# Kernel tuning notes

Measured on AMD Instinct MI355X. Metric: run time of the kernel, lower is better.

Reference implementation:

```python
import jax, jax.numpy as jnp
import numpy as np

N = 100000      # nodes
E = 1600000     # edges
R = 8           # relation types
D = 128         # in_dim = h_dim = out_dim

def setup_inputs() -> dict:
    key = jax.random.key(0)
    ks = jax.random.split(key, 10)
    feats = jax.random.normal(ks[0], (N, D), dtype=jnp.float32)
    src = jax.random.randint(ks[1], (E,), 0, N, dtype=jnp.int32)
    dst = jax.random.randint(ks[2], (E,), 0, N, dtype=jnp.int32)
    etype = jax.random.randint(ks[3], (E,), 0, R, dtype=jnp.int32)
    s = 0.05  # keep activations well-scaled
    W1 = jax.random.normal(ks[4], (R, D, D), dtype=jnp.float32) * s
    loop_w1 = jax.random.normal(ks[5], (D, D), dtype=jnp.float32) * s
    b1 = jnp.zeros((D,), dtype=jnp.float32)
    W2 = jax.random.normal(ks[6], (R, D, D), dtype=jnp.float32) * s
    loop_w2 = jax.random.normal(ks[7], (D, D), dtype=jnp.float32) * s
    b2 = jnp.zeros((D,), dtype=jnp.float32)
    return {"feats": feats, "W1": W1, "loop_w1": loop_w1, "b1": b1,
            "W2": W2, "loop_w2": loop_w2, "b2": b2,
            "src": src, "dst": dst, "etype": etype}

def _rel_conv(h, W, loop_w, b, src, dst, etype, relu):
    # Per-relation transform of all node features: [R, N, out]
    # (cheaper than gathering a per-edge [E, in, out] weight tensor)
    h_rel = jnp.einsum('ni,rio->rno', h, W)
    # Per-edge message = W_{etype(e)} @ h[src(e)] : [E, out]
    msg = h_rel[etype, src]
    # Sum-aggregate messages at destination nodes
    agg = jax.ops.segment_sum(msg, dst, num_segments=h.shape[0])
    out = agg + h @ loop_w + b  # self-loop + bias
    return jax.nn.relu(out) if relu else out

def reference(feats, W1, loop_w1, b1, W2, loop_w2, b2, src, dst, etype):
    # eval-mode forward: dropout is identity
    h = _rel_conv(feats, W1, loop_w1, b1, src, dst, etype, relu=True)
    h = _rel_conv(h, W2, loop_w2, b2, src, dst, etype, relu=False)
    return h
```

## Files before the change

### kernel.cpp

```cpp
#include <hip/hip_runtime.h>
#include <hip/hip_bf16.h>


#define D 128
#define KTOT 1152
#define KACC 1024
#define BK 32
#define BSH 9
#define BSZ 512
#define TILE 4096

typedef __attribute__((ext_vector_type(8))) __bf16 bf16x8;
typedef __attribute__((ext_vector_type(8))) unsigned short us8;
typedef __attribute__((ext_vector_type(4))) unsigned short us4;
typedef __attribute__((ext_vector_type(4))) float f32x4;

__device__ __forceinline__ unsigned short f2bf(float f) {
    union { float f; unsigned u; } v; v.f = f;
    unsigned r = v.u + 0x7FFF + ((v.u >> 16) & 1);
    return (unsigned short)(r >> 16);
}
__device__ __forceinline__ float bf2f(unsigned short u) {
    return __uint_as_float((unsigned)u << 16);
}

__device__ __forceinline__ int lds_off(int row, int c) {
    return row * 32 + ((c ^ ((row >> 1) & 3)) << 3);
}


__global__ __launch_bounds__(256) void histA_kernel(const int* __restrict__ dst,
                                                    int* __restrict__ bcnt, int E, int nbuck) {
    __shared__ int c[1024];
    int t = threadIdx.x;
    for (int i = t; i < nbuck; i += 256) c[i] = 0;
    __syncthreads();
    int stride = gridDim.x * 256;
    for (int e = blockIdx.x * 256 + t; e < E; e += stride)
        atomicAdd(&c[dst[e] >> BSH], 1);
    __syncthreads();
    for (int i = t; i < nbuck; i += 256)
        if (c[i]) atomicAdd(&bcnt[i], c[i]);
}

__global__ __launch_bounds__(1024) void scanA_kernel(const int* __restrict__ bcnt,
                                                     int* __restrict__ boffs,
                                                     int* __restrict__ bhead, int nbuck) {
    int t = threadIdx.x;
    int v = (t < nbuck) ? bcnt[t] : 0;
    int lane = t & 63, w = t >> 6;
    int inc = v;
    #pragma unroll
    for (int off = 1; off < 64; off <<= 1) {
        int n = __shfl_up(inc, off, 64);
        if (lane >= off) inc += n;
    }
    __shared__ int ws[16];
    if (lane == 63) ws[w] = inc;
    __syncthreads();
    int wbase = 0;
    for (int i = 0; i < w; ++i) wbase += ws[i];
    int ex = wbase + inc - v;
    if (t < nbuck) { boffs[t] = ex; bhead[t] = ex; }
    if (t == nbuck - 1) boffs[nbuck] = ex + v;
}

__global__ __launch_bounds__(1024) void scatterA_kernel(const int* __restrict__ src,
                                                        const int* __restrict__ dst,
                                                        const int* __restrict__ et,
                                                        int* __restrict__ bhead,
                                                        int* __restrict__ sortedA, int E, int nbuck) {
    __shared__ int skey[TILE];
    __shared__ unsigned char sbkt[TILE];
    __shared__ int cnt[256];
    __shared__ int lpos[256];
    __shared__ int gdelta[256];
    __shared__ int ws[4];
    const int t = threadIdx.x;
    const int e0 = blockIdx.x * TILE;
    int dreg[4];

    if (t < 256) cnt[t] = 0;
    __syncthreads();
    #pragma unroll
    for (int j = 0; j < 4; ++j) {
        int e = e0 + j * 1024 + t;
        int d = -1;
        if (e < E) { d = dst[e]; atomicAdd(&cnt[d >> BSH], 1); }
        dreg[j] = d;
    }
    __syncthreads();
    int c = 0, inc = 0;
    const int lane = t & 63, w = t >> 6;
    if (t < 256) {
        c = cnt[t];
        inc = c;
        #pragma unroll
        for (int off = 1; off < 64; off <<= 1) {
            int n = __shfl_up(inc, off, 64);
            if (lane >= off) inc += n;
        }
        if (lane == 63) ws[w] = inc;
    }
    __syncthreads();
    if (t < 256) {
        int wbase = 0;
        for (int i = 0; i < w; ++i) wbase += ws[i];
        int ex = wbase + inc - c;
        lpos[t] = ex;
        if (c) gdelta[t] = atomicAdd(&bhead[t], c) - ex;
    }
    __syncthreads();
    #pragma unroll
    for (int j = 0; j < 4; ++j) {
        int e = e0 + j * 1024 + t;
        if (e < E) {
            int d = dreg[j];
            int b = d >> BSH;
            int key = ((d & (BSZ - 1)) << 20) | (et[e] << 17) | src[e];
            int p = atomicAdd(&lpos[b], 1);
            skey[p] = key;
            sbkt[p] = (unsigned char)b;
        }
    }
    __syncthreads();
    int ntile = min(TILE, E - e0);
    for (int i = t; i < ntile; i += 1024)
        sortedA[gdelta[sbkt[i]] + i] = skey[i];
}


__global__ __launch_bounds__(256) void passB_kernel(const int* __restrict__ sortedA,
                                                    const int* __restrict__ boffs,
                                                    int* __restrict__ sorted,
                                                    int* __restrict__ offs2,
                                                    int N8, int E, int nbuck) {
    __shared__ int cnt[4096];
    __shared__ int cur[4096];
    __shared__ int ws[4];
    const int b = blockIdx.x;
    const int t = threadIdx.x;
    const int gb0 = boffs[b], gb1 = boffs[b + 1];
    #pragma unroll
    for (int i = 0; i < 16; ++i) cnt[i * 256 + t] = 0;
    __syncthreads();
    for (int e = gb0 + t; e < gb1; e += 256) {
        int k = sortedA[e];
        atomicAdd(&cnt[(k >> 17) & 4095], 1);
    }
    __syncthreads();
    const int base = t * 16;
    int s = 0;
    #pragma unroll
    for (int i = 0; i < 16; ++i) s += cnt[base + i];
    int lane = t & 63, w = t >> 6;
    int inc = s;
    #pragma unroll
    for (int off = 1; off < 64; off <<= 1) {
        int n = __shfl_up(inc, off, 64);
        if (lane >= off) inc += n;
    }
    if (lane == 63) ws[w] = inc;
    __syncthreads();
    int wbase = 0;
    for (int i = 0; i < w; ++i) wbase += ws[i];
    int run = gb0 + wbase + inc - s;
    int g0 = (b << 12) + base;
    #pragma unroll
    for (int i = 0; i < 16; ++i) {
        int cv = cnt[base + i];
        cur[base + i] = run;
        if (g0 + i <= N8) offs2[g0 + i] = run;
        run += cv;
    }
    __syncthreads();
    for (int e = gb0 + t; e < gb1; e += 256) {
        int k = sortedA[e];
        int p = atomicAdd(&cur[(k >> 17) & 4095], 1);
        sorted[p] = k;
    }
}


__global__ void cast_kernel(const float* __restrict__ W1, const float* __restrict__ lw1,
                            const float* __restrict__ W2, const float* __restrict__ lw2,
                            const float* __restrict__ feats,
                            unsigned short* __restrict__ Bt1, unsigned short* __restrict__ Bt2,
                            unsigned short* __restrict__ hb0, int n4) {
    const int per = KTOT * D;
    int idx = blockIdx.x * blockDim.x + threadIdx.x;
    if (idx < 2 * per) {
        int layer = idx / per;
        int rem = idx - layer * per;
        int k = rem >> 7;
        int o = rem & 127;
        const float* W  = layer ? W2 : W1;
        const float* lw = layer ? lw2 : lw1;
        float val = (k < 1024) ? W[k * D + o] : lw[(k - 1024) * D + o];
        unsigned short* Bt = layer ? Bt2 : Bt1;
        Bt[o * KTOT + k] = f2bf(val);
    } else {
        int i = idx - 2 * per;
        if (i < n4) {
            float4 v = *(const float4*)(feats + (size_t)i * 4);
            us4 o; o.x = f2bf(v.x); o.y = f2bf(v.y); o.z = f2bf(v.z); o.w = f2bf(v.w);
            *(us4*)(hb0 + (size_t)i * 4) = o;
        }
    }
}


__global__ __launch_bounds__(256) void aggregate_kernel(const unsigned short* __restrict__ hb,
                                                        const int* __restrict__ offs2,
                                                        const int* __restrict__ sorted,
                                                        unsigned short* __restrict__ A,
                                                        int v0, int vend) {
    const int t = threadIdx.x;
    const int c = (t & 15) * 8;
    const int gu = blockIdx.x * 16 + (t >> 4);
    const int v = v0 + (gu >> 3);
    const int r = gu & 7;
    if (v >= vend) return;

    const int e0 = offs2[v * 8 + r];
    const int e1 = offs2[v * 8 + r + 1];

    float a0[8], a1[8];
    #pragma unroll
    for (int j = 0; j < 8; ++j) { a0[j] = 0.f; a1[j] = 0.f; }

    int e = e0;
    for (; e + 1 < e1; e += 2) {
        int p0 = sorted[e], p1 = sorted[e + 1];
        us8 h0 = *(const us8*)(hb + (size_t)(p0 & 131071) * D + c);
        us8 h1 = *(const us8*)(hb + (size_t)(p1 & 131071) * D + c);
        #pragma unroll
        for (int j = 0; j < 8; ++j) { a0[j] += bf2f(h0[j]); a1[j] += bf2f(h1[j]); }
    }
    if (e < e1) {
        int p0 = sorted[e];
        us8 h0 = *(const us8*)(hb + (size_t)(p0 & 131071) * D + c);
        #pragma unroll
        for (int j = 0; j < 8; ++j) a0[j] += bf2f(h0[j]);
    }

    us8 o;
    #pragma unroll
    for (int j = 0; j < 8; ++j) o[j] = f2bf(a0[j] + a1[j]);
    *(us8*)(A + (size_t)(v - v0) * KACC + r * 128 + c) = o;
}


__global__ __launch_bounds__(256) void gemm_kernel(const unsigned short* __restrict__ A,
                                                   const unsigned short* __restrict__ hbA,
                                                   const unsigned short* __restrict__ Bt,
                                                   const float* __restrict__ bias,
                                                   float* __restrict__ outf,
                                                   unsigned short* __restrict__ outb,
                                                   int v0, int vend, int relu_bf) {
    __shared__ unsigned short Alds[64 * 32];
    __shared__ unsigned short Blds[128 * 32];
    const int t = threadIdx.x;
    const int lane = t & 63;
    const int w = t >> 6;
    const int quad = lane >> 4;
    const int c16 = lane & 15;
    const int blockRow0 = v0 + blockIdx.x * 64;

    const int srow = t >> 2;
    const int schunk = t & 3;

    f32x4 acc[8];
    #pragma unroll
    for (int j = 0; j < 8; ++j) acc[j] = f32x4{0.f, 0.f, 0.f, 0.f};

    const int aRow = blockRow0 + srow;
    const bool aval = aRow < vend;
    const us8 zz = {0, 0, 0, 0, 0, 0, 0, 0};
    const unsigned short* Arow = A + (size_t)(aRow - v0) * KACC + schunk * 8;
    const unsigned short* Hrow = hbA + (size_t)aRow * D + schunk * 8;
    const unsigned short* Brow0 = Bt + (size_t)srow * KTOT + schunk * 8;
    const unsigned short* Brow1 = Bt + (size_t)(srow + 64) * KTOT + schunk * 8;

    us8 av = zz;
    if (aval) av = *(const us8*)(Arow);
    us8 bv0 = *(const us8*)(Brow0);
    us8 bv1 = *(const us8*)(Brow1);

    for (int k0 = 0; k0 < KTOT; k0 += BK) {
        us8 na = zz, nb0 = zz, nb1 = zz;
        const int kn = k0 + BK;
        if (kn < KTOT) {
            if (aval) {
                if (kn < KACC) na = *(const us8*)(Arow + kn);
                else           na = *(const us8*)(Hrow + (kn - KACC));
            }
            nb0 = *(const us8*)(Brow0 + kn);
            nb1 = *(const us8*)(Brow1 + kn);
        }
        __syncthreads();
        *(us8*)(Alds + lds_off(srow, schunk)) = av;
        *(us8*)(Blds + lds_off(srow,      schunk)) = bv0;
        *(us8*)(Blds + lds_off(srow + 64, schunk)) = bv1;
        __syncthreads();

        bf16x8 af = *(const bf16x8*)(Alds + lds_off(w * 16 + c16, quad));
        #pragma unroll
        for (int ct = 0; ct < 8; ++ct) {
            bf16x8 bfr = *(const bf16x8*)(Blds + lds_off(ct * 16 + c16, quad));
            acc[ct] = __builtin_amdgcn_mfma_f32_16x16x32_bf16(af, bfr, acc[ct], 0, 0, 0);
        }
        av = na; bv0 = nb0; bv1 = nb1;
    }

    int row = blockRow0 + w * 16 + quad * 4;
    #pragma unroll
    for (int ct = 0; ct < 8; ++ct) {
        int col = ct * 16 + c16;
        float bcol = bias[col];
        #pragma unroll
        for (int i = 0; i < 4; ++i) {
            int r = row + i;
            if (r < vend) {
                float vv = acc[ct][i] + bcol;
                if (relu_bf) {
                    vv = fmaxf(vv, 0.f);
                    outb[(size_t)r * D + col] = f2bf(vv);
                } else {
                    outf[(size_t)r * D + col] = vv;
                }
            }
        }
    }
}


extern "C" void kernel_launch(void* const* d_in, const int* in_sizes, int n_in,
                              void* d_out, int out_size, void* d_ws, size_t ws_size,
                              hipStream_t stream) {
    const float* feats = (const float*)d_in[0];
    const float* W1    = (const float*)d_in[1];
    const float* lw1   = (const float*)d_in[2];
    const float* b1    = (const float*)d_in[3];
    const float* W2    = (const float*)d_in[4];
    const float* lw2   = (const float*)d_in[5];
    const float* b2    = (const float*)d_in[6];
    const int*   src   = (const int*)d_in[7];
    const int*   dst   = (const int*)d_in[8];
    const int*   etype = (const int*)d_in[9];
    const int N = in_sizes[0] / D;
    const int E = in_sizes[7];
    float* out = (float*)d_out;

    const int ch = (N + 1) / 2;
    const int nbuck = (N + BSZ - 1) >> BSH;

    size_t woff = 0;
    auto take = [&](size_t bytes) -> void* {
        void* p = (char*)d_ws + woff;
        woff += (bytes + 255) & ~(size_t)255;
        return p;
    };
    int* bcnt           = (int*)take((size_t)1024 * 4);
    int* boffs          = (int*)take((size_t)1025 * 4);
    int* bhead          = (int*)take((size_t)1024 * 4);
    int* offs2          = (int*)take((size_t)(N * 8 + 1) * 4);
    int* sortedA        = (int*)take((size_t)E * 4);
    int* sorted         = (int*)take((size_t)E * 4);
    unsigned short* Bt1 = (unsigned short*)take((size_t)KTOT * D * 2);
    unsigned short* Bt2 = (unsigned short*)take((size_t)KTOT * D * 2);
    unsigned short* hb0 = (unsigned short*)take((size_t)N * D * 2);
    unsigned short* hb1 = (unsigned short*)take((size_t)N * D * 2);
    unsigned short* ACC = (unsigned short*)take((size_t)ch * KACC * 2);

    (void)hipMemsetAsync(bcnt, 0, (size_t)nbuck * 4, stream);

    histA_kernel<<<1024, 256, 0, stream>>>(dst, bcnt, E, nbuck);
    scanA_kernel<<<1, 1024, 0, stream>>>(bcnt, boffs, bhead, nbuck);
    scatterA_kernel<<<(E + TILE - 1) / TILE, 1024, 0, stream>>>(src, dst, etype, bhead, sortedA, E, nbuck);
    passB_kernel<<<nbuck, 256, 0, stream>>>(sortedA, boffs, sorted, offs2, N * 8, E, nbuck);

    int n4 = N * D / 4;
    int cb = (2 * KTOT * D + n4 + 255) / 256;
    cast_kernel<<<cb, 256, 0, stream>>>(W1, lw1, W2, lw2, feats, Bt1, Bt2, hb0, n4);

    for (int layer = 0; layer < 2; ++layer) {
        const unsigned short* hin = layer ? hb1 : hb0;
        const unsigned short* Bt  = layer ? Bt2 : Bt1;
        const float* bias         = layer ? b2  : b1;
        for (int c0 = 0; c0 < N; c0 += ch) {
            int c1 = (c0 + ch < N) ? (c0 + ch) : N;
            int len = c1 - c0;
            int ab = (len * 8 + 15) / 16;
            int gb = (len + 63) / 64;
            aggregate_kernel<<<ab, 256, 0, stream>>>(hin, offs2, sorted, ACC, c0, c1);
            gemm_kernel<<<gb, 256, 0, stream>>>(ACC, hin, Bt, bias, out, hb1, c0, c1, 1 - layer);
        }
    }
}
```

Before: 530.9 us.

## Fuse per-relation aggregation and GEMM into one kernel with LDS-resident A tile

Replaces the separate aggregate and GEMM kernels, and their chunked global ACC buffer, with one fused kernel per layer. Each block aggregates 16 nodes' per-relation sums into shared memory and then runs MFMA against B fragments loaded directly from global memory. This removes the round trip of the large intermediate matrix through HBM and cuts the number of launches. The costs are a 64-float accumulator per thread (register pressure), no LDS staging of B, 16-row tiles that reuse B poorly, and a serial per-thread edge loop that may reduce memory-level parallelism.

New measurement: 832.4 us. +56.8%, slower.

```diff
diff --git a/kernel.cpp b/kernel.cpp
--- a/kernel.cpp
+++ b/kernel.cpp
@@ -4,8 +4,6 @@
 
 #define D 128
 #define KTOT 1152
-#define KACC 1024
-#define BK 32
 #define BSH 9
 #define BSZ 512
 #define TILE 4096
@@ -24,8 +22,8 @@
     return __uint_as_float((unsigned)u << 16);
 }
 
-__device__ __forceinline__ int lds_off(int row, int c) {
-    return row * 32 + ((c ^ ((row >> 1) & 3)) << 3);
+__device__ __forceinline__ int aoff(int row, int rr, int c4) {
+    return (row * 144 + rr * 16 + (c4 ^ ((row + rr) & 15))) * 8;
 }
 
 
@@ -210,118 +208,90 @@
 }
 
 
-__global__ __launch_bounds__(256) void aggregate_kernel(const unsigned short* __restrict__ hb,
-                                                        const int* __restrict__ offs2,
-                                                        const int* __restrict__ sorted,
-                                                        unsigned short* __restrict__ A,
-                                                        int v0, int vend) {
+__global__ __launch_bounds__(256, 4) void fused_kernel(const unsigned short* __restrict__ hb,
+                                                       const int* __restrict__ offs2,
+                                                       const int* __restrict__ sorted,
+                                                       const unsigned short* __restrict__ Bt,
+                                                       const float* __restrict__ bias,
+                                                       float* __restrict__ outf,
+                                                       unsigned short* __restrict__ outb,
+                                                       int N, int relu_bf) {
+    __shared__ unsigned short Asl[16 * 144 * 8];
     const int t = threadIdx.x;
-    const int c = (t & 15) * 8;
-    const int gu = blockIdx.x * 16 + (t >> 4);
-    const int v = v0 + (gu >> 3);
-    const int r = gu & 7;
-    if (v >= vend) return;
-
-    const int e0 = offs2[v * 8 + r];
-    const int e1 = offs2[v * 8 + r + 1];
-
-    float a0[8], a1[8];
-    #pragma unroll
-    for (int j = 0; j < 8; ++j) { a0[j] = 0.f; a1[j] = 0.f; }
-
-    int e = e0;
-    for (; e + 1 < e1; e += 2) {
-        int p0 = sorted[e], p1 = sorted[e + 1];
-        us8 h0 = *(const us8*)(hb + (size_t)(p0 & 131071) * D + c);
-        us8 h1 = *(const us8*)(hb + (size_t)(p1 & 131071) * D + c);
-        #pragma unroll
-        for (int j = 0; j < 8; ++j) { a0[j] += bf2f(h0[j]); a1[j] += bf2f(h1[j]); }
-    }
-    if (e < e1) {
-        int p0 = sorted[e];
-        us8 h0 = *(const us8*)(hb + (size_t)(p0 & 131071) * D + c);
-        #pragma unroll
-        for (int j = 0; j < 8; ++j) a0[j] += bf2f(h0[j]);
-    }
-
-    us8 o;
-    #pragma unroll
-    for (int j = 0; j < 8; ++j) o[j] = f2bf(a0[j] + a1[j]);
-    *(us8*)(A + (size_t)(v - v0) * KACC + r * 128 + c) = o;
-}
-
-
-__global__ __launch_bounds__(256) void gemm_kernel(const unsigned short* __restrict__ A,
-                                                   const unsigned short* __restrict__ hbA,
-                                                   const unsigned short* __restrict__ Bt,
-                                                   const float* __restrict__ bias,
-                                                   float* __restrict__ outf,
-                                                   unsigned short* __restrict__ outb,
-                                                   int v0, int vend, int relu_bf) {
-    __shared__ unsigned short Alds[64 * 32];
-    __shared__ unsigned short Blds[128 * 32];
-    const int t = threadIdx.x;
+    const int v0 = blockIdx.x * 16;
+
+    {
+        const int n = t >> 4;
+        const int sub = t & 15;
+        const int r = sub >> 1;
+        const int half = sub & 1;
+        const int v = v0 + n;
+        int e0 = 0, e1 = 0;
+        if (v < N) { e0 = offs2[v * 8 + r]; e1 = offs2[v * 8 + r + 1]; }
+        float a[64];
+        #pragma unroll
+        for (int j = 0; j < 64; ++j) a[j] = 0.f;
+        const unsigned short* hbase = hb + half * 64;
+        for (int e = e0; e < e1; ++e) {
+            int s = sorted[e] & 131071;
+            const unsigned short* rowp = hbase + (size_t)s * D;
+            #pragma unroll
+            for (int c4 = 0; c4 < 8; ++c4) {
+                us8 hv = *(const us8*)(rowp + c4 * 8);
+                #pragma unroll
+                for (int j = 0; j < 8; ++j) a[c4 * 8 + j] += bf2f(hv[j]);
+            }
+        }
+        #pragma unroll
+        for (int c4 = 0; c4 < 8; ++c4) {
+            us8 o;
+            #pragma unroll
+            for (int j = 0; j < 8; ++j) o[j] = f2bf(a[c4 * 8 + j]);
+            *(us8*)(Asl + aoff(n, r, half * 8 + c4)) = o;
+        }
+    }
+    {
+        const int n = t >> 4;
+        const int c4 = t & 15;
+        const int v = v0 + n;
+        us8 hv = {0, 0, 0, 0, 0, 0, 0, 0};
+        if (v < N) hv = *(const us8*)(hb + (size_t)v * D + c4 * 8);
+        *(us8*)(Asl + aoff(n, 8, c4)) = hv;
+    }
+    __syncthreads();
+
     const int lane = t & 63;
     const int w = t >> 6;
     const int quad = lane >> 4;
     const int c16 = lane & 15;
-    const int blockRow0 = v0 + blockIdx.x * 64;
-
-    const int srow = t >> 2;
-    const int schunk = t & 3;
-
-    f32x4 acc[8];
-    #pragma unroll
-    for (int j = 0; j < 8; ++j) acc[j] = f32x4{0.f, 0.f, 0.f, 0.f};
-
-    const int aRow = blockRow0 + srow;
-    const bool aval = aRow < vend;
-    const us8 zz = {0, 0, 0, 0, 0, 0, 0, 0};
-    const unsigned short* Arow = A + (size_t)(aRow - v0) * KACC + schunk * 8;
-    const unsigned short* Hrow = hbA + (size_t)aRow * D + schunk * 8;
-    const unsigned short* Brow0 = Bt + (size_t)srow * KTOT + schunk * 8;
-    const unsigned short* Brow1 = Bt + (size_t)(srow + 64) * KTOT + schunk * 8;
-
-    us8 av = zz;
-    if (aval) av = *(const us8*)(Arow);
-    us8 bv0 = *(const us8*)(Brow0);
-    us8 bv1 = *(const us8*)(Brow1);
-
-    for (int k0 = 0; k0 < KTOT; k0 += BK) {
-        us8 na = zz, nb0 = zz, nb1 = zz;
-        const int kn = k0 + BK;
-        if (kn < KTOT) {
-            if (aval) {
-                if (kn < KACC) na = *(const us8*)(Arow + kn);
-                else           na = *(const us8*)(Hrow + (kn - KACC));
-            }
-            nb0 = *(const us8*)(Brow0 + kn);
-            nb1 = *(const us8*)(Brow1 + kn);
-        }
-        __syncthreads();
-        *(us8*)(Alds + lds_off(srow, schunk)) = av;
-        *(us8*)(Blds + lds_off(srow,      schunk)) = bv0;
-        *(us8*)(Blds + lds_off(srow + 64, schunk)) = bv1;
-        __syncthreads();
-
-        bf16x8 af = *(const bf16x8*)(Alds + lds_off(w * 16 + c16, quad));
-        #pragma unroll
-        for (int ct = 0; ct < 8; ++ct) {
-            bf16x8 bfr = *(const bf16x8*)(Blds + lds_off(ct * 16 + c16, quad));
-            acc[ct] = __builtin_amdgcn_mfma_f32_16x16x32_bf16(af, bfr, acc[ct], 0, 0, 0);
-        }
-        av = na; bv0 = nb0; bv1 = nb1;
-    }
-
-    int row = blockRow0 + w * 16 + quad * 4;
-    #pragma unroll
-    for (int ct = 0; ct < 8; ++ct) {
-        int col = ct * 16 + c16;
+    f32x4 acc[2];
+    acc[0] = f32x4{0.f, 0.f, 0.f, 0.f};
+    acc[1] = f32x4{0.f, 0.f, 0.f, 0.f};
+    const unsigned short* B0 = Bt + (size_t)(w * 32 + c16) * KTOT + quad * 8;
+    const unsigned short* B1 = Bt + (size_t)(w * 32 + 16 + c16) * KTOT + quad * 8;
+
+    #pragma unroll
+    for (int rr = 0; rr < 9; ++rr) {
+        #pragma unroll
+        for (int ks = 0; ks < 4; ++ks) {
+            bf16x8 af = *(const bf16x8*)(Asl + aoff(c16, rr, ks * 4 + quad));
+            const int kb = rr * 128 + ks * 32;
+            bf16x8 b0 = *(const bf16x8*)(B0 + kb);
+            bf16x8 b1 = *(const bf16x8*)(B1 + kb);
+            acc[0] = __builtin_amdgcn_mfma_f32_16x16x32_bf16(af, b0, acc[0], 0, 0, 0);
+            acc[1] = __builtin_amdgcn_mfma_f32_16x16x32_bf16(af, b1, acc[1], 0, 0, 0);
+        }
+    }
+
+    int row0 = v0 + quad * 4;
+    #pragma unroll
+    for (int ct = 0; ct < 2; ++ct) {
+        int col = w * 32 + ct * 16 + c16;
         float bcol = bias[col];
         #pragma unroll
         for (int i = 0; i < 4; ++i) {
-            int r = row + i;
-            if (r < vend) {
+            int r = row0 + i;
+            if (r < N) {
                 float vv = acc[ct][i] + bcol;
                 if (relu_bf) {
                     vv = fmaxf(vv, 0.f);
@@ -352,7 +322,6 @@
     const int E = in_sizes[7];
     float* out = (float*)d_out;
 
-    const int ch = (N + 1) / 2;
     const int nbuck = (N + BSZ - 1) >> BSH;
 
     size_t woff = 0;
@@ -371,7 +340,6 @@
     unsigned short* Bt2 = (unsigned short*)take((size_t)KTOT * D * 2);
     unsigned short* hb0 = (unsigned short*)take((size_t)N * D * 2);
     unsigned short* hb1 = (unsigned short*)take((size_t)N * D * 2);
-    unsigned short* ACC = (unsigned short*)take((size_t)ch * KACC * 2);
 
     (void)hipMemsetAsync(bcnt, 0, (size_t)nbuck * 4, stream);
 
@@ -384,17 +352,7 @@
     int cb = (2 * KTOT * D + n4 + 255) / 256;
     cast_kernel<<<cb, 256, 0, stream>>>(W1, lw1, W2, lw2, feats, Bt1, Bt2, hb0, n4);
 
-    for (int layer = 0; layer < 2; ++layer) {
-        const unsigned short* hin = layer ? hb1 : hb0;
-        const unsigned short* Bt  = layer ? Bt2 : Bt1;
-        const float* bias         = layer ? b2  : b1;
-        for (int c0 = 0; c0 < N; c0 += ch) {
-            int c1 = (c0 + ch < N) ? (c0 + ch) : N;
-            int len = c1 - c0;
-            int ab = (len * 8 + 15) / 16;
-            int gb = (len + 63) / 64;
-            aggregate_kernel<<<ab, 256, 0, stream>>>(hin, offs2, sorted, ACC, c0, c1);
-            gemm_kernel<<<gb, 256, 0, stream>>>(ACC, hin, Bt, bias, out, hb1, c0, c1, 1 - layer);
-        }
-    }
-}
+    int fb = (N + 15) / 16;
+    fused_kernel<<<fb, 256, 0, stream>>>(hb0, offs2, sorted, Bt1, b1, nullptr, hb1, N, 1);
+    fused_kernel<<<fb, 256, 0, stream>>>(hb1, offs2, sorted, Bt2, b2, out, nullptr, N, 0);
+}
```

## Drop LDS staging in GEMM and load MFMA fragments directly from global memory

Applied to the files above, without the earlier changes.

The GEMM kernel no longer stages A and B tiles through shared memory with double-buffered registers and two barriers per K step. Each wave now owns a 32-column slice of the output and loads its A and B MFMA fragments straight from global memory, computing a 64x32 tile with 4x2 accumulators. This removes the LDS writes and reads and the __syncthreads calls. In exchange, A rows are reloaded by all four waves (relying on L1/L2 for reuse), global loads are strided per lane, and out-of-range rows are clamped instead of zero-filled.

Result: slower. 780.8 us (+47.0%).

```diff
diff --git a/kernel.cpp b/kernel.cpp
--- a/kernel.cpp
+++ b/kernel.cpp
@@ -22,10 +22,6 @@
 }
 __device__ __forceinline__ float bf2f(unsigned short u) {
     return __uint_as_float((unsigned)u << 16);
-}
-
-__device__ __forceinline__ int lds_off(int row, int c) {
-    return row * 32 + ((c ^ ((row >> 1) & 3)) << 3);
 }
 
 
@@ -258,8 +254,6 @@
                                                    float* __restrict__ outf,
                                                    unsigned short* __restrict__ outb,
                                                    int v0, int vend, int relu_bf) {
-    __shared__ unsigned short Alds[64 * 32];
-    __shared__ unsigned short Blds[128 * 32];
     const int t = threadIdx.x;
     const int lane = t & 63;
     const int w = t >> 6;
@@ -267,67 +261,87 @@
     const int c16 = lane & 15;
     const int blockRow0 = v0 + blockIdx.x * 64;
 
-    const int srow = t >> 2;
-    const int schunk = t & 3;
-
-    f32x4 acc[8];
-    #pragma unroll
-    for (int j = 0; j < 8; ++j) acc[j] = f32x4{0.f, 0.f, 0.f, 0.f};
-
-    const int aRow = blockRow0 + srow;
-    const bool aval = aRow < vend;
-    const us8 zz = {0, 0, 0, 0, 0, 0, 0, 0};
-    const unsigned short* Arow = A + (size_t)(aRow - v0) * KACC + schunk * 8;
-    const unsigned short* Hrow = hbA + (size_t)aRow * D + schunk * 8;
-    const unsigned short* Brow0 = Bt + (size_t)srow * KTOT + schunk * 8;
-    const unsigned short* Brow1 = Bt + (size_t)(srow + 64) * KTOT + schunk * 8;
-
-    us8 av = zz;
-    if (aval) av = *(const us8*)(Arow);
-    us8 bv0 = *(const us8*)(Brow0);
-    us8 bv1 = *(const us8*)(Brow1);
-
-    for (int k0 = 0; k0 < KTOT; k0 += BK) {
-        us8 na = zz, nb0 = zz, nb1 = zz;
-        const int kn = k0 + BK;
-        if (kn < KTOT) {
-            if (aval) {
-                if (kn < KACC) na = *(const us8*)(Arow + kn);
-                else           na = *(const us8*)(Hrow + (kn - KACC));
-            }
-            nb0 = *(const us8*)(Brow0 + kn);
-            nb1 = *(const us8*)(Brow1 + kn);
-        }
-        __syncthreads();
-        *(us8*)(Alds + lds_off(srow, schunk)) = av;
-        *(us8*)(Blds + lds_off(srow,      schunk)) = bv0;
-        *(us8*)(Blds + lds_off(srow + 64, schunk)) = bv1;
-        __syncthreads();
-
-        bf16x8 af = *(const bf16x8*)(Alds + lds_off(w * 16 + c16, quad));
+    f32x4 acc[4][2];
+    #pragma unroll
+    for (int rg = 0; rg < 4; ++rg) {
+        acc[rg][0] = f32x4{0.f, 0.f, 0.f, 0.f};
+        acc[rg][1] = f32x4{0.f, 0.f, 0.f, 0.f};
+    }
+
+    const unsigned short* Ap0; const unsigned short* Ap1;
+    const unsigned short* Ap2; const unsigned short* Ap3;
+    const unsigned short* Hp0; const unsigned short* Hp1;
+    const unsigned short* Hp2; const unsigned short* Hp3;
+    {
+        int r0 = min(blockRow0 +  0 + c16, vend - 1);
+        int r1 = min(blockRow0 + 16 + c16, vend - 1);
+        int r2 = min(blockRow0 + 32 + c16, vend - 1);
+        int r3 = min(blockRow0 + 48 + c16, vend - 1);
+        Ap0 = A + (size_t)(r0 - v0) * KACC + quad * 8;
+        Ap1 = A + (size_t)(r1 - v0) * KACC + quad * 8;
+        Ap2 = A + (size_t)(r2 - v0) * KACC + quad * 8;
+        Ap3 = A + (size_t)(r3 - v0) * KACC + quad * 8;
+        Hp0 = hbA + (size_t)r0 * D + quad * 8;
+        Hp1 = hbA + (size_t)r1 * D + quad * 8;
+        Hp2 = hbA + (size_t)r2 * D + quad * 8;
+        Hp3 = hbA + (size_t)r3 * D + quad * 8;
+    }
+    const unsigned short* Bp0 = Bt + (size_t)(w * 32 + c16) * KTOT + quad * 8;
+    const unsigned short* Bp1 = Bt + (size_t)(w * 32 + 16 + c16) * KTOT + quad * 8;
+
+    #pragma unroll 4
+    for (int k0 = 0; k0 < KACC; k0 += BK) {
+        bf16x8 b0 = *(const bf16x8*)(Bp0 + k0);
+        bf16x8 b1 = *(const bf16x8*)(Bp1 + k0);
+        bf16x8 a0 = *(const bf16x8*)(Ap0 + k0);
+        bf16x8 a1 = *(const bf16x8*)(Ap1 + k0);
+        bf16x8 a2 = *(const bf16x8*)(Ap2 + k0);
+        bf16x8 a3 = *(const bf16x8*)(Ap3 + k0);
+        acc[0][0] = __builtin_amdgcn_mfma_f32_16x16x32_bf16(a0, b0, acc[0][0], 0, 0, 0);
+        acc[0][1] = __builtin_amdgcn_mfma_f32_16x16x32_bf16(a0, b1, acc[0][1], 0, 0, 0);
+        acc[1][0] = __builtin_amdgcn_mfma_f32_16x16x32_bf16(a1, b0, acc[1][0], 0, 0, 0);
+        acc[1][1] = __builtin_amdgcn_mfma_f32_16x16x32_bf16(a1, b1, acc[1][1], 0, 0, 0);
+        acc[2][0] = __builtin_amdgcn_mfma_f32_16x16x32_bf16(a2, b0, acc[2][0], 0, 0, 0);
+        acc[2][1] = __builtin_amdgcn_mfma_f32_16x16x32_bf16(a2, b1, acc[2][1], 0, 0, 0);
+        acc[3][0] = __builtin_amdgcn_mfma_f32_16x16x32_bf16(a3, b0, acc[3][0], 0, 0, 0);
+        acc[3][1] = __builtin_amdgcn_mfma_f32_16x16x32_bf16(a3, b1, acc[3][1], 0, 0, 0);
+    }
+    #pragma unroll
+    for (int k0 = 0; k0 < D; k0 += BK) {
+        bf16x8 b0 = *(const bf16x8*)(Bp0 + KACC + k0);
+        bf16x8 b1 = *(const bf16x8*)(Bp1 + KACC + k0);
+        bf16x8 a0 = *(const bf16x8*)(Hp0 + k0);
+        bf16x8 a1 = *(const bf16x8*)(Hp1 + k0);
+        bf16x8 a2 = *(const bf16x8*)(Hp2 + k0);
+        bf16x8 a3 = *(const bf16x8*)(Hp3 + k0);
+        acc[0][0] = __builtin_amdgcn_mfma_f32_16x16x32_bf16(a0, b0, acc[0][0], 0, 0, 0);
+        acc[0][1] = __builtin_amdgcn_mfma_f32_16x16x32_bf16(a0, b1, acc[0][1], 0, 0, 0);
+        acc[1][0] = __builtin_amdgcn_mfma_f32_16x16x32_bf16(a1, b0, acc[1][0], 0, 0, 0);
+        acc[1][1] = __builtin_amdgcn_mfma_f32_16x16x32_bf16(a1, b1, acc[1][1], 0, 0, 0);
+        acc[2][0] = __builtin_amdgcn_mfma_f32_16x16x32_bf16(a2, b0, acc[2][0], 0, 0, 0);
+        acc[2][1] = __builtin_amdgcn_mfma_f32_16x16x32_bf16(a2, b1, acc[2][1], 0, 0, 0);
+        acc[3][0] = __builtin_amdgcn_mfma_f32_16x16x32_bf16(a3, b0, acc[3][0], 0, 0, 0);
+        acc[3][1] = __builtin_amdgcn_mfma_f32_16x16x32_bf16(a3, b1, acc[3][1], 0, 0, 0);
+    }
+
+    #pragma unroll
+    for (int rg = 0; rg < 4; ++rg) {
+        int row = blockRow0 + rg * 16 + quad * 4;
         #pragma unroll
-        for (int ct = 0; ct < 8; ++ct) {
-            bf16x8 bfr = *(const bf16x8*)(Blds + lds_off(ct * 16 + c16, quad));
-            acc[ct] = __builtin_amdgcn_mfma_f32_16x16x32_bf16(af, bfr, acc[ct], 0, 0, 0);
-        }
-        av = na; bv0 = nb0; bv1 = nb1;
-    }
-
-    int row = blockRow0 + w * 16 + quad * 4;
-    #pragma unroll
-    for (int ct = 0; ct < 8; ++ct) {
-        int col = ct * 16 + c16;
-        float bcol = bias[col];
-        #pragma unroll
-        for (int i = 0; i < 4; ++i) {
-            int r = row + i;
-            if (r < vend) {
-                float vv = acc[ct][i] + bcol;
-                if (relu_bf) {
-                    vv = fmaxf(vv, 0.f);
-                    outb[(size_t)r * D + col] = f2bf(vv);
-                } else {
-                    outf[(size_t)r * D + col] = vv;
+        for (int ct = 0; ct < 2; ++ct) {
+            int col = w * 32 + ct * 16 + c16;
+            float bcol = bias[col];
+            #pragma unroll
+            for (int i = 0; i < 4; ++i) {
+                int r = row + i;
+                if (r < vend) {
+                    float vv = acc[rg][ct][i] + bcol;
+                    if (relu_bf) {
+                        vv = fmaxf(vv, 0.f);
+                        outb[(size_t)r * D + col] = f2bf(vv);
+                    } else {
+                        outf[(size_t)r * D + col] = vv;
+                    }
                 }
             }
         }
```
